# Kernel optimization log

Measured on AMD Instinct MI355X. Metric: run time of the kernel, lower is better.

The kernel has to match this reference:

```python
import jax, jax.numpy as jnp
import numpy as np

DIM = 192
HEADS = 6
WS = 12       # window_size
STRIDE = 3    # dilation stride for mask


def build_mask():
    # Static (ws*ws, ws*ws) additive mask: only neighbors with dh%stride==0 and
    # dw%stride==0 are allowed, self (0,0) excluded.
    coords = np.stack(np.meshgrid(np.arange(WS), np.arange(WS), indexing='ij'))
    coords = coords.reshape(2, -1)                       # (2, ws*ws)
    rel = coords[:, :, None] - coords[:, None, :]        # (2, N, N)
    valid = (rel[0] % STRIDE == 0) & (rel[1] % STRIDE == 0)
    valid &= ~((rel[0] == 0) & (rel[1] == 0))
    mask = np.where(valid, 0.0, -np.inf).astype(np.float32)
    return jnp.asarray(mask)


def setup_inputs() -> dict:
    key = jax.random.key(0)
    k1, k2, k3 = jax.random.split(key, 3)
    x = jax.random.normal(k1, (4, DIM, 256, 256), dtype=jnp.float32)
    w_qkv = jax.random.normal(k2, (3 * DIM, DIM), dtype=jnp.float32) * 0.02
    w_proj = jax.random.normal(k3, (DIM, DIM), dtype=jnp.float32) * 0.02
    return {"x": x, "w_qkv": w_qkv, "w_proj": w_proj}


def reference(x, w_qkv, w_proj):
    B, C, H, W = x.shape
    mask = build_mask()                                   # (N, N), N = WS*WS
    pad_r = (WS - W % WS) % WS
    pad_b = (WS - H % WS) % WS
    x = jnp.pad(x, ((0, 0), (0, 0), (0, pad_b), (0, pad_r)), mode='reflect')
    Hp, Wp = x.shape[2], x.shape[3]
    nh, nw = Hp // WS, Wp // WS
    # b c h w -> b h w c -> (b nh nw, ws*ws, c)
    xw = x.transpose(0, 2, 3, 1)
    xw = xw.reshape(B, nh, WS, nw, WS, C).transpose(0, 1, 3, 2, 4, 5)
    xw = xw.reshape(B * nh * nw, WS * WS, C)
    qkv = xw @ w_qkv.T                                    # (bw, n, 3C)
    q, k, v = jnp.split(qkv, 3, axis=-1)
    d = C // HEADS
    scale = d ** (-0.5)
    def heads(t):
        return t.reshape(t.shape[0], t.shape[1], HEADS, d).transpose(0, 2, 1, 3)
    q, k, v = heads(q), heads(k), heads(v)                # (bw, h, n, d)
    attn = jnp.einsum('whnd,whmd->whnm', q * scale, k)
    attn = attn + mask[None, None]
    attn = jax.nn.softmax(attn, axis=-1)
    out = jnp.einsum('whnm,whmd->whnd', attn, v)
    out = out.transpose(0, 2, 1, 3).reshape(out.shape[0], WS * WS, C)
    out = out @ w_proj.T
    # merge windows: (b nh nw, ws*ws, c) -> b c Hp Wp
    out = out.reshape(B, nh, nw, WS, WS, C).transpose(0, 1, 3, 2, 4, 5)
    out = out.reshape(B, Hp, Wp, C).transpose(0, 3, 1, 2)
    return out[:, :, :H, :W]
```

## Files before the change

### kernel.cpp

```cpp
#include <hip/hip_runtime.h>
#include <hip/hip_bf16.h>

typedef __bf16 bf16x8 __attribute__((ext_vector_type(8)));
typedef float f32x4 __attribute__((ext_vector_type(4)));
typedef unsigned int u32x4 __attribute__((ext_vector_type(4)));

#define WSZ 12
#define NTOK 144
#define RES 256
#define NHW 22
#define NWIN (4*NHW*NHW)
#define SCALE 0.17677669529663687f
#define XS 200
#define QS 40
#define VTS 152
#define STS 148

#define WQ_ELEMS (576*192)
#define WP_ELEMS (192*192)
#define WS_NEED ((WQ_ELEMS + WP_ELEMS) * 2)

#define OFF_Q  57600
#define OFF_K  (OFF_Q + 2*11520)
#define OFF_VT (OFF_K + 2*11520)
#define OFF_AO (OFF_VT + 2*32*VTS*2)
#define SMEM_BYTES (OFF_AO + 2*NTOK*QS*2)

static __device__ __forceinline__ unsigned f2u(float f) {
    return (unsigned)__builtin_bit_cast(unsigned short, __float2bfloat16(f));
}
static __device__ __forceinline__ unsigned pk2(float a, float b) {
    return f2u(a) | (f2u(b) << 16);
}
static __device__ __forceinline__ bf16x8 ld8(const void* p) {
    return *(const bf16x8*)p;
}
static __device__ __forceinline__ bf16x8 wfrag(const float* p) {
    const float4* p4 = (const float4*)p;
    float4 lo = p4[0], hi = p4[1];
    u32x4 u = { pk2(lo.x, lo.y), pk2(lo.z, lo.w), pk2(hi.x, hi.y), pk2(hi.z, hi.w) };
    return __builtin_bit_cast(bf16x8, u);
}

__global__ __launch_bounds__(256) void conv_w(const float* __restrict__ wq,
                                              const float* __restrict__ wp,
                                              __hip_bfloat16* __restrict__ dst) {
    int i = blockIdx.x * 256 + threadIdx.x;
    if (i < WQ_ELEMS) dst[i] = __float2bfloat16(wq[i]);
    if (i < WP_ELEMS) dst[WQ_ELEMS + i] = __float2bfloat16(wp[i]);
}

template<bool WB>
__global__ __launch_bounds__(768, 3) void wsa_kernel(
    const float* __restrict__ x,
    const float* __restrict__ w_qkv,
    const float* __restrict__ w_proj,
    const __hip_bfloat16* __restrict__ wqb,
    const __hip_bfloat16* __restrict__ wpb,
    float* __restrict__ out)
{
    __shared__ __align__(16) unsigned char smem[SMEM_BYTES];
    __hip_bfloat16 (* const xw)[XS]  = reinterpret_cast<__hip_bfloat16(*)[XS]>(smem);
    float          (* const stg)[STS] = reinterpret_cast<float(*)[STS]>(smem);
    __hip_bfloat16* const vTp = reinterpret_cast<__hip_bfloat16*>(smem + OFF_VT);

    const int tid  = threadIdx.x;
    const int lane = tid & 63;
    const int wv   = tid >> 6;
    const int col  = lane & 15;
    const int grp  = lane >> 4;

    const int wid0 = blockIdx.x;
    const int wid  = (wid0 & 7) * (NWIN / 8) + (wid0 >> 3);
    const int b    = wid / (NHW * NHW);
    const int r0   = wid % (NHW * NHW);
    const int wh   = r0 / NHW;
    const int ww   = r0 % NHW;

    for (int u = tid; u < 24 * NTOK; u += 768) {
        int c8 = u / NTOK;
        int t  = u - c8 * NTOK;
        int ty = t / WSZ, tx = t - ty * WSZ;
        int h = wh * WSZ + ty; if (h >= RES) h = 2 * RES - 2 - h;
        int w = ww * WSZ + tx; if (w >= RES) w = 2 * RES - 2 - w;
        const float* px = x + ((size_t)(b * 192 + c8 * 8) * RES + h) * RES + w;
        u32x4 uv;
        #pragma unroll
        for (int j = 0; j < 4; ++j)
            uv[j] = pk2(px[(size_t)(2 * j) * RES * RES], px[(size_t)(2 * j + 1) * RES * RES]);
        *(u32x4*)&xw[t][c8 * 8] = uv;
    }
    __syncthreads();

    f32x4 pacc[9];
    #pragma unroll
    for (int m = 0; m < 9; ++m) pacc[m] = (f32x4){0.f, 0.f, 0.f, 0.f};

    const int mh   = wv & 1;
    const int n6   = wv >> 1;
    const int kind = n6 >> 1;
    const int h2q  = n6 & 1;
    const int mt0  = mh ? 4 : 0;
    const int nmt  = mh ? 5 : 4;

    auto do_proj = [&](int hpp) {
        #pragma unroll
        for (int h2 = 0; h2 < 2; ++h2) {
            const int hh = hpp * 2 + h2;
            const bf16x8 Bf = WB ? ld8(wpb + (size_t)(wv * 16 + col) * 192 + hh * 32 + grp * 8)
                                 : wfrag(w_proj + (size_t)(wv * 16 + col) * 192 + hh * 32 + grp * 8);
            const __hip_bfloat16 (* const aoPl)[QS] =
                reinterpret_cast<const __hip_bfloat16(*)[QS]>(smem + OFF_AO + h2 * 11520);
            #pragma unroll
            for (int mt = 0; mt < 9; ++mt) {
                const bf16x8 Af = ld8(&aoPl[mt * 16 + col][grp * 8]);
                pacc[mt] = __builtin_amdgcn_mfma_f32_16x16x32_bf16(Af, Bf, pacc[mt], 0, 0, 0);
            }
        }
    };

    for (int hp = 0; hp < 3; ++hp) {
        {
            const int hh    = hp * 2 + h2q;
            const int rbase = kind * 192 + hh * 32;
            f32x4 acc[2][5];
            #pragma unroll
            for (int d = 0; d < 2; ++d)
                #pragma unroll
                for (int m = 0; m < 5; ++m) acc[d][m] = (f32x4){0.f, 0.f, 0.f, 0.f};
            #pragma unroll
            for (int k0 = 0; k0 < 6; ++k0) {
                const bf16x8 B0 = WB ? ld8(wqb + (size_t)(rbase + col) * 192 + k0 * 32 + grp * 8)
                                     : wfrag(w_qkv + (size_t)(rbase + col) * 192 + k0 * 32 + grp * 8);
                const bf16x8 B1 = WB ? ld8(wqb + (size_t)(rbase + 16 + col) * 192 + k0 * 32 + grp * 8)
                                     : wfrag(w_qkv + (size_t)(rbase + 16 + col) * 192 + k0 * 32 + grp * 8);
                #pragma unroll
                for (int m = 0; m < 5; ++m) {
                    if (m < nmt) {
                        const bf16x8 Af = ld8(&xw[(mt0 + m) * 16 + col][k0 * 32 + grp * 8]);
                        acc[0][m] = __builtin_amdgcn_mfma_f32_16x16x32_bf16(Af, B0, acc[0][m], 0, 0, 0);
                        acc[1][m] = __builtin_amdgcn_mfma_f32_16x16x32_bf16(Af, B1, acc[1][m], 0, 0, 0);
                    }
                }
            }
            const float qs = (kind == 0) ? SCALE : 1.f;
            if (kind < 2) {
                __hip_bfloat16 (* const pl)[QS] = reinterpret_cast<__hip_bfloat16(*)[QS]>(
                    smem + (kind == 0 ? OFF_Q : OFF_K) + h2q * 11520);
                #pragma unroll
                for (int m = 0; m < 5; ++m) if (m < nmt) {
                    #pragma unroll
                    for (int r = 0; r < 4; ++r) {
                        const int trow = (mt0 + m) * 16 + grp * 4 + r;
                        pl[trow][col]      = __float2bfloat16(acc[0][m][r] * qs);
                        pl[trow][16 + col] = __float2bfloat16(acc[1][m][r] * qs);
                    }
                }
            } else {
                #pragma unroll
                for (int m = 0; m < 5; ++m) if (m < nmt) {
                    #pragma unroll
                    for (int r = 0; r < 4; ++r) {
                        const int t  = (mt0 + m) * 16 + grp * 4 + r;
                        const int ti = t / WSZ, tj = t - ti * WSZ;
                        const int cs   = (ti % 3) * 3 + (tj % 3);
                        const int ctok = (ti / 3) * 4 + (tj / 3);
                        vTp[(size_t)(h2q * 32 + col) * VTS + cs * 16 + ctok]      = __float2bfloat16(acc[0][m][r]);
                        vTp[(size_t)(h2q * 32 + 16 + col) * VTS + cs * 16 + ctok] = __float2bfloat16(acc[1][m][r]);
                    }
                }
            }
            if (hp > 0) do_proj(hp - 1);
        }
        __syncthreads();

        for (int u = wv; u < 18; u += 12) {
            const int h2 = u / 9;
            const int cs = u % 9;
            __hip_bfloat16 (* const qPl)[QS] = reinterpret_cast<__hip_bfloat16(*)[QS]>(smem + OFF_Q + h2 * 11520);
            __hip_bfloat16 (* const kPl)[QS] = reinterpret_cast<__hip_bfloat16(*)[QS]>(smem + OFF_K + h2 * 11520);
            __hip_bfloat16 (* const aoPl)[QS] = reinterpret_cast<__hip_bfloat16(*)[QS]>(smem + OFF_AO + h2 * 11520);
            const int ci = cs / 3, cj = cs % 3;
            const int tcol = (ci + 3 * (col >> 2)) * WSZ + cj + 3 * (col & 3);
            const bf16x8 Kf = ld8(&kPl[tcol][grp * 8]);
            const bf16x8 Qf = ld8(&qPl[tcol][grp * 8]);
            f32x4 S = {0.f, 0.f, 0.f, 0.f};
            S = __builtin_amdgcn_mfma_f32_16x16x32_bf16(Kf, Qf, S, 0, 0, 0);
            float e[4]; float mx = -1e30f;
            #pragma unroll
            for (int r = 0; r < 4; ++r) {
                float s = (grp * 4 + r == col) ? -1e30f : S[r];
                e[r] = s;
                mx = fmaxf(mx, s);
            }
            mx = fmaxf(mx, __shfl_xor(mx, 16));
            mx = fmaxf(mx, __shfl_xor(mx, 32));
            float sum = 0.f;
            #pragma unroll
            for (int r = 0; r < 4; ++r) { e[r] = __expf(e[r] - mx); sum += e[r]; }
            sum += __shfl_xor(sum, 16);
            sum += __shfl_xor(sum, 32);
            const float inv = 1.f / sum;
            const unsigned w0 = pk2(e[0] * inv, e[1] * inv);
            const unsigned w1 = pk2(e[2] * inv, e[3] * inv);
            u32x4 pa = {0u, 0u, 0u, 0u};
            {
                const int sA = (col + 32 * grp) * 4;
                int q0 = __builtin_amdgcn_ds_bpermute(sA,      (int)w0);
                int q1 = __builtin_amdgcn_ds_bpermute(sA,      (int)w1);
                int q2 = __builtin_amdgcn_ds_bpermute(sA + 64, (int)w0);
                int q3 = __builtin_amdgcn_ds_bpermute(sA + 64, (int)w1);
                if (grp < 2) pa = (u32x4){(unsigned)q0, (unsigned)q1, (unsigned)q2, (unsigned)q3};
            }
            const bf16x8 PB = __builtin_bit_cast(bf16x8, pa);
            #pragma unroll
            for (int d0 = 0; d0 < 2; ++d0) {
                const bf16x8 VA = ld8(&vTp[(size_t)(h2 * 32 + d0 * 16 + col) * VTS + cs * 16 + (grp & 1) * 8]);
                f32x4 O = {0.f, 0.f, 0.f, 0.f};
                O = __builtin_amdgcn_mfma_f32_16x16x32_bf16(VA, PB, O, 0, 0, 0);
                #pragma unroll
                for (int r = 0; r < 4; ++r)
                    aoPl[tcol][d0 * 16 + grp * 4 + r] = __float2bfloat16(O[r]);
            }
        }
        __syncthreads();
    }

    do_proj(2);
    __syncthreads();

    {
        const int ocl = wv * 16 + col;
        #pragma unroll
        for (int mt = 0; mt < 9; ++mt) {
            float4 v4 = make_float4(pacc[mt][0], pacc[mt][1], pacc[mt][2], pacc[mt][3]);
            *(float4*)&stg[ocl][mt * 16 + grp * 4] = v4;
        }
    }
    __syncthreads();
    #pragma unroll
    for (int it = 0; it < 9; ++it) {
        int v = tid + it * 768;
        int seg = v % 3;
        int rest = v / 3;
        int ty = rest % 12;
        int oc = rest / 12;
        int h  = wh * WSZ + ty;
        int w0 = ww * WSZ + seg * 4;
        if (h < RES && w0 < RES) {
            float4 val = *(const float4*)&stg[oc][ty * 12 + seg * 4];
            *(float4*)&out[((size_t)(b * 192 + oc) * RES + h) * RES + w0] = val;
        }
    }
}

extern "C" void kernel_launch(void* const* d_in, const int* in_sizes, int n_in,
                              void* d_out, int out_size, void* d_ws, size_t ws_size,
                              hipStream_t stream) {
    const float* x      = (const float*)d_in[0];
    const float* w_qkv  = (const float*)d_in[1];
    const float* w_proj = (const float*)d_in[2];
    float* out = (float*)d_out;
    if (ws_size >= (size_t)WS_NEED) {
        __hip_bfloat16* wqb = (__hip_bfloat16*)d_ws;
        __hip_bfloat16* wpb = wqb + WQ_ELEMS;
        conv_w<<<dim3((WQ_ELEMS + 255) / 256), dim3(256), 0, stream>>>(w_qkv, w_proj, wqb);
        wsa_kernel<true><<<dim3(NWIN), dim3(768), 0, stream>>>(x, w_qkv, w_proj, wqb, wpb, out);
    } else {
        wsa_kernel<false><<<dim3(NWIN), dim3(768), 0, stream>>>(x, w_qkv, w_proj, nullptr, nullptr, out);
    }
}
```

Baseline: 292.9 us.

## Register-block QKV and projection GEMMs as 3x3 tiles per wave

Both the QKV GEMM and the output projection now give each wave a 3x3 block of 16x16 output tiles, instead of a row strip. This cuts LDS fragment loads per MFMA through register reuse. The QKV GEMM swaps operand roles (weights as A, tokens as B), so Q/K results can be written as packed 8-byte bf16 stores. The attention-output store is vectorized the same way. One barrier before writing the staging buffer is removed, which relies on the staging area not overlapping the attention-output planes. Each wave also issues more global weight fragment loads per k-step.

```diff
diff --git a/kernel.cpp b/kernel.cpp
--- a/kernel.cpp
+++ b/kernel.cpp
@@ -69,6 +69,8 @@
     const int wv   = tid >> 6;
     const int col  = lane & 15;
     const int grp  = lane >> 4;
+    const int wr   = wv & 3;
+    const int tc   = wv >> 2;
 
     const int wid0 = blockIdx.x;
     const int wid  = (wid0 & 7) * (NWIN / 8) + (wid0 >> 3);
@@ -92,81 +94,93 @@
     }
     __syncthreads();
 
-    f32x4 pacc[9];
+    f32x4 pacc[3][3];
     #pragma unroll
-    for (int m = 0; m < 9; ++m) pacc[m] = (f32x4){0.f, 0.f, 0.f, 0.f};
-
-    const int mh   = wv & 1;
-    const int n6   = wv >> 1;
-    const int kind = n6 >> 1;
-    const int h2q  = n6 & 1;
-    const int mt0  = mh ? 4 : 0;
-    const int nmt  = mh ? 5 : 4;
+    for (int jt = 0; jt < 3; ++jt)
+        #pragma unroll
+        for (int io = 0; io < 3; ++io)
+            pacc[jt][io] = (f32x4){0.f, 0.f, 0.f, 0.f};
 
     auto do_proj = [&](int hpp) {
         #pragma unroll
         for (int h2 = 0; h2 < 2; ++h2) {
             const int hh = hpp * 2 + h2;
-            const bf16x8 Bf = WB ? ld8(wpb + (size_t)(wv * 16 + col) * 192 + hh * 32 + grp * 8)
-                                 : wfrag(w_proj + (size_t)(wv * 16 + col) * 192 + hh * 32 + grp * 8);
             const __hip_bfloat16 (* const aoPl)[QS] =
                 reinterpret_cast<const __hip_bfloat16(*)[QS]>(smem + OFF_AO + h2 * 11520);
-            #pragma unroll
-            for (int mt = 0; mt < 9; ++mt) {
-                const bf16x8 Af = ld8(&aoPl[mt * 16 + col][grp * 8]);
-                pacc[mt] = __builtin_amdgcn_mfma_f32_16x16x32_bf16(Af, Bf, pacc[mt], 0, 0, 0);
-            }
+            bf16x8 Bf[3], Af[3];
+            #pragma unroll
+            for (int io = 0; io < 3; ++io)
+                Bf[io] = WB ? ld8(wpb + (size_t)((wr * 3 + io) * 16 + col) * 192 + hh * 32 + grp * 8)
+                            : wfrag(w_proj + (size_t)((wr * 3 + io) * 16 + col) * 192 + hh * 32 + grp * 8);
+            #pragma unroll
+            for (int jt = 0; jt < 3; ++jt)
+                Af[jt] = ld8(&aoPl[(tc * 3 + jt) * 16 + col][grp * 8]);
+            #pragma unroll
+            for (int jt = 0; jt < 3; ++jt)
+                #pragma unroll
+                for (int io = 0; io < 3; ++io)
+                    pacc[jt][io] = __builtin_amdgcn_mfma_f32_16x16x32_bf16(Af[jt], Bf[io], pacc[jt][io], 0, 0, 0);
         }
     };
 
     for (int hp = 0; hp < 3; ++hp) {
         {
-            const int hh    = hp * 2 + h2q;
-            const int rbase = kind * 192 + hh * 32;
-            f32x4 acc[2][5];
-            #pragma unroll
-            for (int d = 0; d < 2; ++d)
-                #pragma unroll
-                for (int m = 0; m < 5; ++m) acc[d][m] = (f32x4){0.f, 0.f, 0.f, 0.f};
-            #pragma unroll
+            f32x4 acc[3][3];
+            #pragma unroll
+            for (int i = 0; i < 3; ++i)
+                #pragma unroll
+                for (int j = 0; j < 3; ++j) acc[i][j] = (f32x4){0.f, 0.f, 0.f, 0.f};
+
+            #pragma unroll 2
             for (int k0 = 0; k0 < 6; ++k0) {
-                const bf16x8 B0 = WB ? ld8(wqb + (size_t)(rbase + col) * 192 + k0 * 32 + grp * 8)
-                                     : wfrag(w_qkv + (size_t)(rbase + col) * 192 + k0 * 32 + grp * 8);
-                const bf16x8 B1 = WB ? ld8(wqb + (size_t)(rbase + 16 + col) * 192 + k0 * 32 + grp * 8)
-                                     : wfrag(w_qkv + (size_t)(rbase + 16 + col) * 192 + k0 * 32 + grp * 8);
-                #pragma unroll
-                for (int m = 0; m < 5; ++m) {
-                    if (m < nmt) {
-                        const bf16x8 Af = ld8(&xw[(mt0 + m) * 16 + col][k0 * 32 + grp * 8]);
-                        acc[0][m] = __builtin_amdgcn_mfma_f32_16x16x32_bf16(Af, B0, acc[0][m], 0, 0, 0);
-                        acc[1][m] = __builtin_amdgcn_mfma_f32_16x16x32_bf16(Af, B1, acc[1][m], 0, 0, 0);
+                bf16x8 Xf[3];
+                #pragma unroll
+                for (int j = 0; j < 3; ++j)
+                    Xf[j] = ld8(&xw[(tc * 3 + j) * 16 + col][k0 * 32 + grp * 8]);
+                #pragma unroll
+                for (int i = 0; i < 3; ++i) {
+                    const int tau  = wr * 3 + i;
+                    const int kind = tau >> 2;
+                    const int h2   = (tau >> 1) & 1;
+                    const int dh   = tau & 1;
+                    const int rg   = kind * 192 + (hp * 2 + h2) * 32 + dh * 16 + col;
+                    const bf16x8 Wf = WB ? ld8(wqb + (size_t)rg * 192 + k0 * 32 + grp * 8)
+                                         : wfrag(w_qkv + (size_t)rg * 192 + k0 * 32 + grp * 8);
+                    #pragma unroll
+                    for (int j = 0; j < 3; ++j)
+                        acc[i][j] = __builtin_amdgcn_mfma_f32_16x16x32_bf16(Wf, Xf[j], acc[i][j], 0, 0, 0);
+                }
+            }
+
+            #pragma unroll
+            for (int i = 0; i < 3; ++i) {
+                const int tau  = wr * 3 + i;
+                const int kind = tau >> 2;
+                const int h2   = (tau >> 1) & 1;
+                const int dh   = tau & 1;
+                if (kind < 2) {
+                    __hip_bfloat16 (* const pl)[QS] = reinterpret_cast<__hip_bfloat16(*)[QS]>(
+                        smem + (kind == 0 ? OFF_Q : OFF_K) + h2 * 11520);
+                    const float qs = (kind == 0) ? SCALE : 1.f;
+                    #pragma unroll
+                    for (int j = 0; j < 3; ++j) {
+                        const int t = (tc * 3 + j) * 16 + col;
+                        uint2 pv;
+                        pv.x = pk2(acc[i][j][0] * qs, acc[i][j][1] * qs);
+                        pv.y = pk2(acc[i][j][2] * qs, acc[i][j][3] * qs);
+                        *(uint2*)&pl[t][dh * 16 + grp * 4] = pv;
                     }
-                }
-            }
-            const float qs = (kind == 0) ? SCALE : 1.f;
-            if (kind < 2) {
-                __hip_bfloat16 (* const pl)[QS] = reinterpret_cast<__hip_bfloat16(*)[QS]>(
-                    smem + (kind == 0 ? OFF_Q : OFF_K) + h2q * 11520);
-                #pragma unroll
-                for (int m = 0; m < 5; ++m) if (m < nmt) {
+                } else {
+                    const int dbase = h2 * 32 + dh * 16 + grp * 4;
                     #pragma unroll
-                    for (int r = 0; r < 4; ++r) {
-                        const int trow = (mt0 + m) * 16 + grp * 4 + r;
-                        pl[trow][col]      = __float2bfloat16(acc[0][m][r] * qs);
-                        pl[trow][16 + col] = __float2bfloat16(acc[1][m][r] * qs);
-                    }
-                }
-            } else {
-                #pragma unroll
-                for (int m = 0; m < 5; ++m) if (m < nmt) {
-                    #pragma unroll
-                    for (int r = 0; r < 4; ++r) {
-                        const int t  = (mt0 + m) * 16 + grp * 4 + r;
+                    for (int j = 0; j < 3; ++j) {
+                        const int t  = (tc * 3 + j) * 16 + col;
                         const int ti = t / WSZ, tj = t - ti * WSZ;
                         const int cs   = (ti % 3) * 3 + (tj % 3);
                         const int ctok = (ti / 3) * 4 + (tj / 3);
-                        vTp[(size_t)(h2q * 32 + col) * VTS + cs * 16 + ctok]      = __float2bfloat16(acc[0][m][r]);
-                        vTp[(size_t)(h2q * 32 + 16 + col) * VTS + cs * 16 + ctok] = __float2bfloat16(acc[1][m][r]);
+                        #pragma unroll
+                        for (int r = 0; r < 4; ++r)
+                            vTp[(size_t)(dbase + r) * VTS + cs * 16 + ctok] = __float2bfloat16(acc[i][j][r]);
                     }
                 }
             }
@@ -218,23 +232,25 @@
                 const bf16x8 VA = ld8(&vTp[(size_t)(h2 * 32 + d0 * 16 + col) * VTS + cs * 16 + (grp & 1) * 8]);
                 f32x4 O = {0.f, 0.f, 0.f, 0.f};
                 O = __builtin_amdgcn_mfma_f32_16x16x32_bf16(VA, PB, O, 0, 0, 0);
-                #pragma unroll
-                for (int r = 0; r < 4; ++r)
-                    aoPl[tcol][d0 * 16 + grp * 4 + r] = __float2bfloat16(O[r]);
+                uint2 ov;
+                ov.x = pk2(O[0], O[1]);
+                ov.y = pk2(O[2], O[3]);
+                *(uint2*)&aoPl[tcol][d0 * 16 + grp * 4] = ov;
             }
         }
         __syncthreads();
     }
 
     do_proj(2);
-    __syncthreads();
-
-    {
-        const int ocl = wv * 16 + col;
-        #pragma unroll
-        for (int mt = 0; mt < 9; ++mt) {
-            float4 v4 = make_float4(pacc[mt][0], pacc[mt][1], pacc[mt][2], pacc[mt][3]);
-            *(float4*)&stg[ocl][mt * 16 + grp * 4] = v4;
+
+    #pragma unroll
+    for (int jt = 0; jt < 3; ++jt) {
+        #pragma unroll
+        for (int io = 0; io < 3; ++io) {
+            const int ocl = (wr * 3 + io) * 16 + col;
+            const int t0  = (tc * 3 + jt) * 16 + grp * 4;
+            float4 v4 = make_float4(pacc[jt][io][0], pacc[jt][io][1], pacc[jt][io][2], pacc[jt][io][3]);
+            *(float4*)&stg[ocl][t0] = v4;
         }
     }
     __syncthreads();
```

Result: slower. 355.6 us (+21.4%).
